# Kernel optimization log

Measured on AMD Instinct MI355X. Metric: run time of the kernel, lower is better.

## Reference

```python
import jax, jax.numpy as jnp
import numpy as np

N = 131072      # total nodes = num_graphs * numNodes
E = 2097152     # edges (avg degree 16)
C_IN = 64
HID = 64        # hiddenChannels
NODES = 128     # numNodes per graph
B = 1024        # num_graphs
NCLS = 4


def setup_inputs() -> dict:
    key = jax.random.key(0)
    ks = jax.random.split(key, 10)
    x = jax.random.normal(ks[0], (N, C_IN), jnp.float32)
    edge_index = jax.random.randint(ks[1], (2, E), 0, N, dtype=jnp.int32)
    edge_attr = jax.random.uniform(ks[2], (E,), jnp.float32)
    # GCNConv params (stored as [in, out]); PyG uses glorot init, bias zeros
    W1 = jax.random.normal(ks[3], (C_IN, 2 * HID), jnp.float32) * (1.0 / np.sqrt(C_IN))
    b1 = jnp.zeros((2 * HID,), jnp.float32)
    W2 = jax.random.normal(ks[4], (2 * HID, HID), jnp.float32) * (1.0 / np.sqrt(2 * HID))
    b2 = jnp.zeros((HID,), jnp.float32)
    Wfc = jax.random.normal(ks[5], (HID * NODES, NCLS), jnp.float32) * (1.0 / np.sqrt(HID * NODES))
    bfc = jnp.zeros((NCLS,), jnp.float32)
    return {"x": x, "edge_index": edge_index, "edge_attr": edge_attr,
            "W1": W1, "b1": b1, "W2": W2, "b2": b2, "Wfc": Wfc, "bfc": bfc}


def gcn_conv(x, src, dst, ew, W, b):
    # PyG GCNConv: add self-loops (weight 1), symmetric normalization,
    # linear transform, scatter-add aggregation at target nodes, + bias.
    loop = jnp.arange(N, dtype=src.dtype)
    s = jnp.concatenate([src, loop])
    d = jnp.concatenate([dst, loop])
    w = jnp.concatenate([ew, jnp.ones((N,), ew.dtype)])
    deg = jax.ops.segment_sum(w, d, num_segments=N)                  # [N]
    dis = jnp.where(deg > 0, jax.lax.rsqrt(jnp.maximum(deg, 1e-30)), 0.0)
    norm = dis[s] * w * dis[d]                                       # [E+N]
    h = x @ W                                                        # [N, out]
    msg = h[s] * norm[:, None]                                       # gather + scale
    out = jax.ops.segment_sum(msg, d, num_segments=N)                # scatter-add
    return out + b


def reference(x, edge_index, edge_attr, W1, b1, W2, b2, Wfc, bfc):
    src, dst = edge_index[0], edge_index[1]
    h = jax.nn.relu(gcn_conv(x, src, dst, edge_attr, W1, b1))
    h = jax.nn.relu(gcn_conv(h, src, dst, edge_attr, W2, b2))
    h = h.reshape(B, HID * NODES)
    logits = h @ Wfc + bfc
    return jax.nn.softmax(logits, axis=1)
```

## Files before the change

### kernel.cpp

```cpp
#include <hip/hip_runtime.h>

#define N_NODES 131072
#define NE      2097152
#define CIN     64
#define HID     64
#define H2X     128
#define NODESG  128
#define NGRAPH  1024
#define NCLS    4

#define NBUCK   256
#define NPB     512
#define HBLK    1024
#define EPB     2048
#define DEGSC   1048576.0f
#define DEGMASK ((1ull << 40) - 1)

typedef short bf16x8 __attribute__((ext_vector_type(8)));
typedef float f32x4  __attribute__((ext_vector_type(4)));

__device__ __forceinline__ unsigned short f2b(float f) {
    unsigned int u = __float_as_uint(f);
    return (unsigned short)((u + 0x7fffu + ((u >> 16) & 1u)) >> 16);
}
__device__ __forceinline__ unsigned int pack2(float a, float b) {
    return (unsigned int)f2b(a) | ((unsigned int)f2b(b) << 16);
}
__device__ __forceinline__ float blo(unsigned u) { return __uint_as_float(u << 16); }
__device__ __forceinline__ float bhi(unsigned u) { return __uint_as_float(u & 0xffff0000u); }


__global__ __launch_bounds__(256) void k_wswiz(
        const float* __restrict__ W1, const float* __restrict__ W2,
        unsigned short* __restrict__ wf1, unsigned short* __restrict__ wf2) {
    int tid = threadIdx.x;
    #pragma unroll
    for (int it = 0; it < 4; ++it) {
        int idx = tid + 256 * it;
        int kt = idx >> 9, nt = (idx >> 6) & 7, l = idx & 63;
        int lm = l & 15, lq = l >> 4;
        unsigned pk[4];
        #pragma unroll
        for (int jp = 0; jp < 4; ++jp) {
            float w0 = W1[(kt*32 + lq*8 + 2*jp)     * H2X + nt*16 + lm];
            float w1 = W1[(kt*32 + lq*8 + 2*jp + 1) * H2X + nt*16 + lm];
            pk[jp] = pack2(w0, w1);
        }
        *(uint4*)&wf1[idx * 8] = make_uint4(pk[0], pk[1], pk[2], pk[3]);
    }
    #pragma unroll
    for (int it = 0; it < 4; ++it) {
        int idx = tid + 256 * it;
        int kt = idx >> 8, nt = (idx >> 6) & 3, l = idx & 63;
        int lm = l & 15, lq = l >> 4;
        unsigned pk[4];
        #pragma unroll
        for (int jp = 0; jp < 4; ++jp) {
            float w0 = W2[(kt*32 + lq*8 + 2*jp)     * HID + nt*16 + lm];
            float w1 = W2[(kt*32 + lq*8 + 2*jp + 1) * HID + nt*16 + lm];
            pk[jp] = pack2(w0, w1);
        }
        *(uint4*)&wf2[idx * 8] = make_uint4(pk[0], pk[1], pk[2], pk[3]);
    }
}


__global__ __launch_bounds__(256) void k_hist(const int* __restrict__ dst,
                                              int* __restrict__ hist) {
    __shared__ unsigned bh[NBUCK];
    int t = threadIdx.x;
    bh[t] = 0;
    __syncthreads();
    int base = blockIdx.x * EPB;
    #pragma unroll
    for (int k = 0; k < EPB / 256; ++k) {
        int d = dst[base + t + 256 * k];
        atomicAdd(&bh[d >> 9], 1u);
    }
    __syncthreads();
    hist[t * HBLK + blockIdx.x] = (int)bh[t];
}

__global__ void k_scan1(const int* __restrict__ in, int* __restrict__ out,
                        int* __restrict__ partial) {
    __shared__ int sd[256];
    int t = threadIdx.x;
    int base = blockIdx.x * 512;
    int c0 = in[base + 2*t];
    int c1 = in[base + 2*t + 1];
    int loc = c0 + c1;
    sd[t] = loc;
    __syncthreads();
    for (int off = 1; off < 256; off <<= 1) {
        int v = (t >= off) ? sd[t - off] : 0;
        __syncthreads();
        sd[t] += v;
        __syncthreads();
    }
    int excl = sd[t] - loc;
    out[base + 2*t]     = excl;
    out[base + 2*t + 1] = excl + c0;
    if (t == 255) partial[blockIdx.x] = sd[t];
}

__global__ void k_scan2(int* __restrict__ partial) {
    __shared__ int sd[256];
    int t = threadIdx.x;
    int p0 = partial[2*t], p1 = partial[2*t + 1];
    int loc = p0 + p1;
    sd[t] = loc;
    __syncthreads();
    for (int off = 1; off < 256; off <<= 1) {
        int v = (t >= off) ? sd[t - off] : 0;
        __syncthreads();
        sd[t] += v;
        __syncthreads();
    }
    int excl = sd[t] - loc;
    partial[2*t]     = excl;
    partial[2*t + 1] = excl + p0;
}

__global__ __launch_bounds__(256) void k_scatter(
        const int* __restrict__ src, const int* __restrict__ dst,
        const float* __restrict__ ew, const int* __restrict__ hist,
        const int* __restrict__ partial, unsigned long long* __restrict__ part) {
    __shared__ unsigned lcur[NBUCK];
    int t = threadIdx.x;
    int gi = t * HBLK + blockIdx.x;
    lcur[t] = (unsigned)(hist[gi] + partial[gi >> 9]);
    __syncthreads();
    int base = blockIdx.x * EPB;
    #pragma unroll
    for (int k = 0; k < EPB / 256; ++k) {
        int e = base + t + 256 * k;
        int s = src[e], d = dst[e];
        unsigned w = __float_as_uint(ew[e]);
        unsigned p = atomicAdd(&lcur[d >> 9], 1u);
        part[p] = ((unsigned long long)w << 32) |
                  ((unsigned long long)(unsigned)(d & 511) << 17) |
                  (unsigned long long)(unsigned)s;
    }
}

__global__ __launch_bounds__(256) void k_bucket(
        const unsigned long long* __restrict__ part, const int* __restrict__ hist,
        const int* __restrict__ partial, int2* __restrict__ csr,
        int* __restrict__ rowptr, int* __restrict__ counts, float* __restrict__ dis) {
    __shared__ unsigned long long dc[NPB];
    __shared__ unsigned cnt2[NPB];
    __shared__ int rp[NPB];
    __shared__ int sd[256];
    int t = threadIdx.x, b = blockIdx.x;
    dc[t] = 0; dc[t + 256] = 0;
    cnt2[t] = 0; cnt2[t + 256] = 0;
    __syncthreads();
    int start = hist[b * HBLK] + partial[2 * b];
    int end   = (b == NBUCK - 1) ? NE : (hist[(b + 1) * HBLK] + partial[2 * (b + 1)]);

    for (int j = start + t; j < end; j += 256) {
        unsigned long long p = part[j];
        unsigned dl = (unsigned)(p >> 17) & 511u;
        float w = __uint_as_float((unsigned)(p >> 32));
        atomicAdd(&dc[dl], (1ull << 40) | (unsigned long long)(unsigned)(w * DEGSC));
    }
    __syncthreads();

    unsigned long long d0 = dc[2*t], d1 = dc[2*t + 1];
    int c0 = (int)(d0 >> 40), c1 = (int)(d1 >> 40);
    int loc = c0 + c1;
    sd[t] = loc;
    __syncthreads();
    for (int off = 1; off < 256; off <<= 1) {
        int v = (t >= off) ? sd[t - off] : 0;
        __syncthreads();
        sd[t] += v;
        __syncthreads();
    }
    int excl = sd[t] - loc;
    rp[2*t] = excl; rp[2*t + 1] = excl + c0;

    int n0 = b * NPB;
    rowptr[n0 + 2*t]     = start + excl;
    rowptr[n0 + 2*t + 1] = start + excl + c0;
    counts[n0 + 2*t]     = c0;
    counts[n0 + 2*t + 1] = c1;
    float dg0 = (float)(d0 & DEGMASK) * (1.0f / DEGSC);
    float dg1 = (float)(d1 & DEGMASK) * (1.0f / DEGSC);
    dis[n0 + 2*t]     = rsqrtf(dg0 + 1.0f);
    dis[n0 + 2*t + 1] = rsqrtf(dg1 + 1.0f);
    __syncthreads();

    for (int j = start + t; j < end; j += 256) {
        unsigned long long p = part[j];
        unsigned dl = (unsigned)(p >> 17) & 511u;
        int s = (int)(p & 0x1ffffu);
        unsigned r = atomicAdd(&cnt2[dl], 1u);
        csr[start + rp[dl] + (int)r] = make_int2(s, (int)(unsigned)(p >> 32));
    }
}

__global__ void k_xcast(const float* __restrict__ x, const float* __restrict__ dis,
                        uint2* __restrict__ xb2) {
    int i = blockIdx.x * blockDim.x + threadIdx.x;
    float d = dis[i >> 4];
    float4 v = ((const float4*)x)[i];
    xb2[i] = make_uint2(pack2(d * v.x, d * v.y), pack2(d * v.z, d * v.w));
}


#define GATHER_PAIR(TAB, pA, pB, nA, nB, cmA, cmB, a0,a1,a2,a3, b0,b1,b2,b3, vSA, vSB) \
    {                                                                                  \
        int   sA0 = __shfl(pA.x, qid),      sA1 = __shfl(pA.x, qid + 4);               \
        int   sA2 = __shfl(pA.x, qid + 8),  sA3 = __shfl(pA.x, qid + 12);              \
        float fA0 = __int_as_float(__shfl(pA.y, qid));                                 \
        float fA1 = __int_as_float(__shfl(pA.y, qid + 4));                             \
        float fA2 = __int_as_float(__shfl(pA.y, qid + 8));                             \
        float fA3 = __int_as_float(__shfl(pA.y, qid + 12));                            \
        int   sB0 = __shfl(pB.x, qid),      sB1 = __shfl(pB.x, qid + 4);               \
        int   sB2 = __shfl(pB.x, qid + 8),  sB3 = __shfl(pB.x, qid + 12);              \
        float fB0 = __int_as_float(__shfl(pB.y, qid));                                 \
        float fB1 = __int_as_float(__shfl(pB.y, qid + 4));                             \
        float fB2 = __int_as_float(__shfl(pB.y, qid + 8));                             \
        float fB3 = __int_as_float(__shfl(pB.y, qid + 12));                            \
        uint2 vA0 = TAB[((unsigned)sA0 << 4) | ql];                                    \
        uint2 vA1 = TAB[((unsigned)sA1 << 4) | ql];                                    \
        uint2 vA2 = TAB[((unsigned)sA2 << 4) | ql];                                    \
        uint2 vA3 = TAB[((unsigned)sA3 << 4) | ql];                                    \
        uint2 vB0 = TAB[((unsigned)sB0 << 4) | ql];                                    \
        uint2 vB1 = TAB[((unsigned)sB1 << 4) | ql];                                    \
        uint2 vB2 = TAB[((unsigned)sB2 << 4) | ql];                                    \
        uint2 vB3 = TAB[((unsigned)sB3 << 4) | ql];                                    \
        vSA = TAB[((unsigned)nA << 4) | ql];                                           \
        vSB = TAB[((unsigned)nB << 4) | ql];                                           \
        a0 = fmaf(fA0, blo(vA0.x), a0); a1 = fmaf(fA0, bhi(vA0.x), a1);                \
        a2 = fmaf(fA0, blo(vA0.y), a2); a3 = fmaf(fA0, bhi(vA0.y), a3);                \
        a0 = fmaf(fA1, blo(vA1.x), a0); a1 = fmaf(fA1, bhi(vA1.x), a1);                \
        a2 = fmaf(fA1, blo(vA1.y), a2); a3 = fmaf(fA1, bhi(vA1.y), a3);                \
        a0 = fmaf(fA2, blo(vA2.x), a0); a1 = fmaf(fA2, bhi(vA2.x), a1);                \
        a2 = fmaf(fA2, blo(vA2.y), a2); a3 = fmaf(fA2, bhi(vA2.y), a3);                \
        a0 = fmaf(fA3, blo(vA3.x), a0); a1 = fmaf(fA3, bhi(vA3.x), a1);                \
        a2 = fmaf(fA3, blo(vA3.y), a2); a3 = fmaf(fA3, bhi(vA3.y), a3);                \
        b0 = fmaf(fB0, blo(vB0.x), b0); b1 = fmaf(fB0, bhi(vB0.x), b1);                \
        b2 = fmaf(fB0, blo(vB0.y), b2); b3 = fmaf(fB0, bhi(vB0.y), b3);                \
        b0 = fmaf(fB1, blo(vB1.x), b0); b1 = fmaf(fB1, bhi(vB1.x), b1);                \
        b2 = fmaf(fB1, blo(vB1.y), b2); b3 = fmaf(fB1, bhi(vB1.y), b3);                \
        b0 = fmaf(fB2, blo(vB2.x), b0); b1 = fmaf(fB2, bhi(vB2.x), b1);                \
        b2 = fmaf(fB2, blo(vB2.y), b2); b3 = fmaf(fB2, bhi(vB2.y), b3);                \
        b0 = fmaf(fB3, blo(vB3.x), b0); b1 = fmaf(fB3, bhi(vB3.x), b1);                \
        b2 = fmaf(fB3, blo(vB3.y), b2); b3 = fmaf(fB3, bhi(vB3.y), b3);                \
        int tsA = (cmA > 16) ? ((cmA - 13) >> 2) : 0;                                  \
        for (int k = 0; k < tsA; ++k) {                                                \
            int jj = 16 + 4 * k + qid;                                                 \
            int   s = __shfl(pA.x, jj);                                                \
            float f = __int_as_float(__shfl(pA.y, jj));                                \
            uint2 v = TAB[((unsigned)s << 4) | ql];                                    \
            a0 = fmaf(f, blo(v.x), a0); a1 = fmaf(f, bhi(v.x), a1);                    \
            a2 = fmaf(f, blo(v.y), a2); a3 = fmaf(f, bhi(v.y), a3);                    \
        }                                                                              \
        int tsB = (cmB > 16) ? ((cmB - 13) >> 2) : 0;                                  \
        for (int k = 0; k < tsB; ++k) {                                                \
            int jj = 16 + 4 * k + qid;                                                 \
            int   s = __shfl(pB.x, jj);                                                \
            float f = __int_as_float(__shfl(pB.y, jj));                                \
            uint2 v = TAB[((unsigned)s << 4) | ql];                                    \
            b0 = fmaf(f, blo(v.x), b0); b1 = fmaf(f, bhi(v.x), b1);                    \
            b2 = fmaf(f, blo(v.y), b2); b3 = fmaf(f, bhi(v.y), b3);                    \
        }                                                                              \
        a0 += __shfl_xor(a0, 16); a1 += __shfl_xor(a1, 16);                            \
        a2 += __shfl_xor(a2, 16); a3 += __shfl_xor(a3, 16);                            \
        a0 += __shfl_xor(a0, 32); a1 += __shfl_xor(a1, 32);                            \
        a2 += __shfl_xor(a2, 32); a3 += __shfl_xor(a3, 32);                            \
        b0 += __shfl_xor(b0, 16); b1 += __shfl_xor(b1, 16);                            \
        b2 += __shfl_xor(b2, 16); b3 += __shfl_xor(b3, 16);                            \
        b0 += __shfl_xor(b0, 32); b1 += __shfl_xor(b1, 32);                            \
        b2 += __shfl_xor(b2, 32); b3 += __shfl_xor(b3, 32);                            \
    }


__global__ __launch_bounds__(256, 4) void k_layer1(
        const uint2* __restrict__ xb2, const int2* __restrict__ csr,
        const int* __restrict__ rowptr, const int* __restrict__ counts,
        const float* __restrict__ dis, const unsigned short* __restrict__ wf1,
        const unsigned short* __restrict__ wf2, const float* __restrict__ b1,
        unsigned short* __restrict__ t2u) {
    __shared__ unsigned short sagg_b[32][72];
    __shared__ unsigned short sh1[32][136];
    __shared__ float sb[H2X];
    int tid = threadIdx.x;
    if (tid < H2X) sb[tid] = b1[tid];

    int wave = tid >> 6, lane = tid & 63;
    int qid = lane >> 4, ql = lane & 15;
    int n0 = blockIdx.x * 32;
    int nb = n0 + wave * 8;

    int cm8[8], cnt8[8], rs8[8];
    float dn8[8];
    int2 myp[8];
    #pragma unroll
    for (int i = 0; i < 8; ++i) {
        rs8[i] = rowptr[nb + i];
        cnt8[i] = counts[nb + i];
        dn8[i] = dis[nb + i];
        cm8[i] = cnt8[i] < 64 ? cnt8[i] : 64;
    }
    #pragma unroll
    for (int i = 0; i < 8; ++i)
        myp[i] = (lane < cm8[i]) ? csr[rs8[i] + lane] : make_int2(0, 0);

    #pragma unroll
    for (int ip = 0; ip < 8; ip += 2) {
        int2 pA = myp[ip], pB = myp[ip + 1];
        int nA = nb + ip, nB = nA + 1;
        float a0 = 0.f, a1 = 0.f, a2 = 0.f, a3 = 0.f;
        float b0 = 0.f, b1v = 0.f, b2v = 0.f, b3 = 0.f;
        uint2 vSA, vSB;
        GATHER_PAIR(xb2, pA, pB, nA, nB, cm8[ip], cm8[ip + 1],
                    a0, a1, a2, a3, b0, b1v, b2v, b3, vSA, vSB);
        for (int jj = 64; jj < cnt8[ip]; ++jj) {
            int2 p = csr[rs8[ip] + jj];
            float f = __int_as_float(p.y);
            uint2 v = xb2[((unsigned)p.x << 4) | ql];
            if (qid == 0) {
                a0 += f * blo(v.x); a1 += f * bhi(v.x);
                a2 += f * blo(v.y); a3 += f * bhi(v.y);
            }
        }
        for (int jj = 64; jj < cnt8[ip + 1]; ++jj) {
            int2 p = csr[rs8[ip + 1] + jj];
            float f = __int_as_float(p.y);
            uint2 v = xb2[((unsigned)p.x << 4) | ql];
            if (qid == 0) {
                b0 += f * blo(v.x); b1v += f * bhi(v.x);
                b2v += f * blo(v.y); b3 += f * bhi(v.y);
            }
        }
        if (qid == 0) {
            float dnA = dn8[ip], dnB = dn8[ip + 1];
            int m = wave * 8 + ip;
            *(uint2*)&sagg_b[m][ql * 4] =
                make_uint2(pack2(dnA * (a0 + blo(vSA.x)), dnA * (a1 + bhi(vSA.x))),
                           pack2(dnA * (a2 + blo(vSA.y)), dnA * (a3 + bhi(vSA.y))));
            *(uint2*)&sagg_b[m + 1][ql * 4] =
                make_uint2(pack2(dnB * (b0 + blo(vSB.x)), dnB * (b1v + bhi(vSB.x))),
                           pack2(dnB * (b2v + blo(vSB.y)), dnB * (b3 + bhi(vSB.y))));
        }
    }
    __syncthreads();

    int mt = wave & 1, ntb = (wave >> 1) * 4;
    int lm = lane & 15, lq = lane >> 4;
    bf16x8 af0 = *(const bf16x8*)&sagg_b[mt*16 + lm][lq * 8];
    bf16x8 af1 = *(const bf16x8*)&sagg_b[mt*16 + lm][32 + lq * 8];
    #pragma unroll
    for (int t = 0; t < 4; ++t) {
        int nt = ntb + t;
        bf16x8 bf0 = *(const bf16x8*)&wf1[(nt*64 + lane) * 8];
        bf16x8 bf1 = *(const bf16x8*)&wf1[((8 + nt)*64 + lane) * 8];
        f32x4 acc = {0.f, 0.f, 0.f, 0.f};
        acc = __builtin_amdgcn_mfma_f32_16x16x32_bf16(af0, bf0, acc, 0, 0, 0);
        acc = __builtin_amdgcn_mfma_f32_16x16x32_bf16(af1, bf1, acc, 0, 0, 0);
        int ch = nt*16 + lm;
        float bias = sb[ch];
        #pragma unroll
        for (int r = 0; r < 4; ++r)
            sh1[mt*16 + lq*4 + r][ch] = f2b(fmaxf(acc[r] + bias, 0.f));
    }
    __syncthreads();

    #pragma unroll
    for (int ti = 0; ti < 2; ++ti) {
        int t = wave * 2 + ti;
        int mt2 = t & 1, nt2 = t >> 1;
        f32x4 acc = {0.f, 0.f, 0.f, 0.f};
        #pragma unroll
        for (int kt = 0; kt < 4; ++kt) {
            bf16x8 af = *(const bf16x8*)&sh1[mt2*16 + lm][kt*32 + lq*8];
            bf16x8 bf = *(const bf16x8*)&wf2[((kt*4 + nt2)*64 + lane) * 8];
            acc = __builtin_amdgcn_mfma_f32_16x16x32_bf16(af, bf, acc, 0, 0, 0);
        }
        int ch = nt2*16 + lm;
        #pragma unroll
        for (int r = 0; r < 4; ++r) {
            int node = n0 + mt2*16 + lq*4 + r;
            t2u[(size_t)node * HID + ch] = f2b(dis[node] * acc[r]);
        }
    }
}


__global__ __launch_bounds__(256, 4) void k_agg2(
        const uint2* __restrict__ t2y, const int2* __restrict__ csr,
        const int* __restrict__ rowptr, const int* __restrict__ counts,
        const float* __restrict__ dis, const float* __restrict__ b2,
        unsigned short* __restrict__ h2b) {
    int tid = threadIdx.x;
    int wave = tid >> 6, lane = tid & 63;
    int qid = lane >> 4, ql = lane & 15;
    float4 bb = *(const float4*)&b2[ql * 4];
    int n0 = blockIdx.x * 32;
    int nb = n0 + wave * 8;

    int cm8[8], cnt8[8], rs8[8];
    float dn8[8];
    int2 myp[8];
    #pragma unroll
    for (int i = 0; i < 8; ++i) {
        rs8[i] = rowptr[nb + i];
        cnt8[i] = counts[nb + i];
        dn8[i] = dis[nb + i];
        cm8[i] = cnt8[i] < 64 ? cnt8[i] : 64;
    }
    #pragma unroll
    for (int i = 0; i < 8; ++i)
        myp[i] = (lane < cm8[i]) ? csr[rs8[i] + lane] : make_int2(0, 0);

    #pragma unroll
    for (int ip = 0; ip < 8; ip += 2) {
        int2 pA = myp[ip], pB = myp[ip + 1];
        int nA = nb + ip, nB = nA + 1;
        float a0 = 0.f, a1 = 0.f, a2 = 0.f, a3 = 0.f;
        float b0 = 0.f, b1v = 0.f, b2v = 0.f, b3 = 0.f;
        uint2 vSA, vSB;
        GATHER_PAIR(t2y, pA, pB, nA, nB, cm8[ip], cm8[ip + 1],
                    a0, a1, a2, a3, b0, b1v, b2v, b3, vSA, vSB);
        for (int jj = 64; jj < cnt8[ip]; ++jj) {
            int2 p = csr[rs8[ip] + jj];
            float f = __int_as_float(p.y);
            uint2 v = t2y[((unsigned)p.x << 4) | ql];
            if (qid == 0) {
                a0 += f * blo(v.x); a1 += f * bhi(v.x);
                a2 += f * blo(v.y); a3 += f * bhi(v.y);
            }
        }
        for (int jj = 64; jj < cnt8[ip + 1]; ++jj) {
            int2 p = csr[rs8[ip + 1] + jj];
            float f = __int_as_float(p.y);
            uint2 v = t2y[((unsigned)p.x << 4) | ql];
            if (qid == 0) {
                b0 += f * blo(v.x); b1v += f * bhi(v.x);
                b2v += f * blo(v.y); b3 += f * bhi(v.y);
            }
        }
        if (qid == 0) {
            float dnA = dn8[ip], dnB = dn8[ip + 1];
            float oa0 = fmaxf(fmaf(dnA, a0 + blo(vSA.x), bb.x), 0.f);
            float oa1 = fmaxf(fmaf(dnA, a1 + bhi(vSA.x), bb.y), 0.f);
            float oa2 = fmaxf(fmaf(dnA, a2 + blo(vSA.y), bb.z), 0.f);
            float oa3 = fmaxf(fmaf(dnA, a3 + bhi(vSA.y), bb.w), 0.f);
            float ob0 = fmaxf(fmaf(dnB, b0 + blo(vSB.x), bb.x), 0.f);
            float ob1 = fmaxf(fmaf(dnB, b1v + bhi(vSB.x), bb.y), 0.f);
            float ob2 = fmaxf(fmaf(dnB, b2v + blo(vSB.y), bb.z), 0.f);
            float ob3 = fmaxf(fmaf(dnB, b3 + bhi(vSB.y), bb.w), 0.f);
            *(uint2*)&h2b[((unsigned)nA << 6) | (ql * 4)] =
                make_uint2(pack2(oa0, oa1), pack2(oa2, oa3));
            *(uint2*)&h2b[((unsigned)nB << 6) | (ql * 4)] =
                make_uint2(pack2(ob0, ob1), pack2(ob2, ob3));
        }
    }
}


__global__ __launch_bounds__(256) void k_fc(
        const unsigned short* __restrict__ h2b, const float* __restrict__ Wfc,
        const float* __restrict__ bfc, float* __restrict__ out) {
    __shared__ float4 red[256];
    int b = blockIdx.x, t = threadIdx.x;
    const uint2* hrow = (const uint2*)(h2b + (size_t)b * (HID * NODESG));
    const float4* W4 = (const float4*)Wfc;
    float4 a = make_float4(0.f, 0.f, 0.f, 0.f);
    #pragma unroll
    for (int j = 0; j < 8; ++j) {
        int i = j * 256 + t;
        uint2 hv = hrow[i];
        float h0 = blo(hv.x), h1 = bhi(hv.x), h2v = blo(hv.y), h3 = bhi(hv.y);
        float4 w0 = W4[i * 4 + 0];
        float4 w1 = W4[i * 4 + 1];
        float4 w2 = W4[i * 4 + 2];
        float4 w3 = W4[i * 4 + 3];
        a.x = fmaf(h0, w0.x, a.x); a.y = fmaf(h0, w0.y, a.y);
        a.z = fmaf(h0, w0.z, a.z); a.w = fmaf(h0, w0.w, a.w);
        a.x = fmaf(h1, w1.x, a.x); a.y = fmaf(h1, w1.y, a.y);
        a.z = fmaf(h1, w1.z, a.z); a.w = fmaf(h1, w1.w, a.w);
        a.x = fmaf(h2v, w2.x, a.x); a.y = fmaf(h2v, w2.y, a.y);
        a.z = fmaf(h2v, w2.z, a.z); a.w = fmaf(h2v, w2.w, a.w);
        a.x = fmaf(h3, w3.x, a.x); a.y = fmaf(h3, w3.y, a.y);
        a.z = fmaf(h3, w3.z, a.z); a.w = fmaf(h3, w3.w, a.w);
    }
    red[t] = a;
    __syncthreads();
    for (int s = 128; s > 0; s >>= 1) {
        if (t < s) {
            red[t].x += red[t + s].x; red[t].y += red[t + s].y;
            red[t].z += red[t + s].z; red[t].w += red[t + s].w;
        }
        __syncthreads();
    }
    if (t == 0) {
        float l0 = red[0].x + bfc[0];
        float l1 = red[0].y + bfc[1];
        float l2 = red[0].z + bfc[2];
        float l3 = red[0].w + bfc[3];
        float mx = fmaxf(fmaxf(l0, l1), fmaxf(l2, l3));
        float e0 = expf(l0 - mx), e1 = expf(l1 - mx);
        float e2 = expf(l2 - mx), e3 = expf(l3 - mx);
        float inv = 1.f / (e0 + e1 + e2 + e3);
        float4 o = make_float4(e0 * inv, e1 * inv, e2 * inv, e3 * inv);
        *(float4*)&out[(size_t)b * 4] = o;
    }
}


extern "C" void kernel_launch(void* const* d_in, const int* in_sizes, int n_in,
                              void* d_out, int out_size, void* d_ws, size_t ws_size,
                              hipStream_t stream) {
    const float* x   = (const float*)d_in[0];
    const int*   ei  = (const int*)  d_in[1];
    const float* ea  = (const float*)d_in[2];
    const float* W1  = (const float*)d_in[3];
    const float* b1  = (const float*)d_in[4];
    const float* W2  = (const float*)d_in[5];
    const float* b2  = (const float*)d_in[6];
    const float* Wfc = (const float*)d_in[7];
    const float* bfc = (const float*)d_in[8];
    float* out = (float*)d_out;
    const int* src = ei;
    const int* dst = ei + NE;

    char* ws = (char*)d_ws;
    size_t off = 0;
    int*   hist   = (int*)  (ws + off); off += (size_t)NBUCK * HBLK * 4;
    int*   partial= (int*)  (ws + off); off += 4096;
    int*   counts = (int*)  (ws + off); off += (size_t)N_NODES * 4;
    int*   rowptr = (int*)  (ws + off); off += (size_t)N_NODES * 4;
    float* dis    = (float*)(ws + off); off += (size_t)N_NODES * 4;
    unsigned short* wf1 = (unsigned short*)(ws + off); off += 8192 * 2;
    unsigned short* wf2 = (unsigned short*)(ws + off); off += 8192 * 2;
    int2*  csr    = (int2*) (ws + off); off += (size_t)NE * 8;
    uint2* xb2    = (uint2*)(ws + off); off += (size_t)N_NODES * CIN * 2;
    unsigned short* t2u = (unsigned short*)(ws + off); off += (size_t)N_NODES * HID * 2;
    unsigned short* h2b = (unsigned short*)(ws + off); off += (size_t)N_NODES * HID * 2;
    unsigned long long* part = (unsigned long long*)t2u;

    hipMemsetAsync(hist, 0, (size_t)NBUCK * HBLK * 4 + 4096, stream);

    k_wswiz  <<<1, 256, 0, stream>>>(W1, W2, wf1, wf2);
    k_hist   <<<HBLK, 256, 0, stream>>>(dst, hist);
    k_scan1  <<<NBUCK * HBLK / 512, 256, 0, stream>>>(hist, hist, partial);
    k_scan2  <<<1, 256, 0, stream>>>(partial);
    k_scatter<<<HBLK, 256, 0, stream>>>(src, dst, ea, hist, partial, part);
    k_bucket <<<NBUCK, 256, 0, stream>>>(part, hist, partial, csr, rowptr, counts, dis);
    k_xcast  <<<(N_NODES * CIN / 4) / 256, 256, 0, stream>>>(x, dis, xb2);
    k_layer1 <<<N_NODES / 32, 256, 0, stream>>>(xb2, csr, rowptr, counts, dis,
                                                wf1, wf2, b1, t2u);
    k_agg2   <<<N_NODES / 32, 256, 0, stream>>>((const uint2*)t2u, csr, rowptr,
                                                counts, dis, b2, h2b);
    k_fc     <<<NGRAPH, 256, 0, stream>>>(h2b, Wfc, bfc, out);
}
```

Baseline: 267.4 us.

## Software-pipeline neighbor gathers across node pairs in aggregation kernels

```diff
diff --git a/kernel.cpp b/kernel.cpp
--- a/kernel.cpp
+++ b/kernel.cpp
@@ -209,72 +209,49 @@
 }
 
 
-#define GATHER_PAIR(TAB, pA, pB, nA, nB, cmA, cmB, a0,a1,a2,a3, b0,b1,b2,b3, vSA, vSB) \
-    {                                                                                  \
-        int   sA0 = __shfl(pA.x, qid),      sA1 = __shfl(pA.x, qid + 4);               \
-        int   sA2 = __shfl(pA.x, qid + 8),  sA3 = __shfl(pA.x, qid + 12);              \
-        float fA0 = __int_as_float(__shfl(pA.y, qid));                                 \
-        float fA1 = __int_as_float(__shfl(pA.y, qid + 4));                             \
-        float fA2 = __int_as_float(__shfl(pA.y, qid + 8));                             \
-        float fA3 = __int_as_float(__shfl(pA.y, qid + 12));                            \
-        int   sB0 = __shfl(pB.x, qid),      sB1 = __shfl(pB.x, qid + 4);               \
-        int   sB2 = __shfl(pB.x, qid + 8),  sB3 = __shfl(pB.x, qid + 12);              \
-        float fB0 = __int_as_float(__shfl(pB.y, qid));                                 \
-        float fB1 = __int_as_float(__shfl(pB.y, qid + 4));                             \
-        float fB2 = __int_as_float(__shfl(pB.y, qid + 8));                             \
-        float fB3 = __int_as_float(__shfl(pB.y, qid + 12));                            \
-        uint2 vA0 = TAB[((unsigned)sA0 << 4) | ql];                                    \
-        uint2 vA1 = TAB[((unsigned)sA1 << 4) | ql];                                    \
-        uint2 vA2 = TAB[((unsigned)sA2 << 4) | ql];                                    \
-        uint2 vA3 = TAB[((unsigned)sA3 << 4) | ql];                                    \
-        uint2 vB0 = TAB[((unsigned)sB0 << 4) | ql];                                    \
-        uint2 vB1 = TAB[((unsigned)sB1 << 4) | ql];                                    \
-        uint2 vB2 = TAB[((unsigned)sB2 << 4) | ql];                                    \
-        uint2 vB3 = TAB[((unsigned)sB3 << 4) | ql];                                    \
-        vSA = TAB[((unsigned)nA << 4) | ql];                                           \
-        vSB = TAB[((unsigned)nB << 4) | ql];                                           \
-        a0 = fmaf(fA0, blo(vA0.x), a0); a1 = fmaf(fA0, bhi(vA0.x), a1);                \
-        a2 = fmaf(fA0, blo(vA0.y), a2); a3 = fmaf(fA0, bhi(vA0.y), a3);                \
-        a0 = fmaf(fA1, blo(vA1.x), a0); a1 = fmaf(fA1, bhi(vA1.x), a1);                \
-        a2 = fmaf(fA1, blo(vA1.y), a2); a3 = fmaf(fA1, bhi(vA1.y), a3);                \
-        a0 = fmaf(fA2, blo(vA2.x), a0); a1 = fmaf(fA2, bhi(vA2.x), a1);                \
-        a2 = fmaf(fA2, blo(vA2.y), a2); a3 = fmaf(fA2, bhi(vA2.y), a3);                \
-        a0 = fmaf(fA3, blo(vA3.x), a0); a1 = fmaf(fA3, bhi(vA3.x), a1);                \
-        a2 = fmaf(fA3, blo(vA3.y), a2); a3 = fmaf(fA3, bhi(vA3.y), a3);                \
-        b0 = fmaf(fB0, blo(vB0.x), b0); b1 = fmaf(fB0, bhi(vB0.x), b1);                \
-        b2 = fmaf(fB0, blo(vB0.y), b2); b3 = fmaf(fB0, bhi(vB0.y), b3);                \
-        b0 = fmaf(fB1, blo(vB1.x), b0); b1 = fmaf(fB1, bhi(vB1.x), b1);                \
-        b2 = fmaf(fB1, blo(vB1.y), b2); b3 = fmaf(fB1, bhi(vB1.y), b3);                \
-        b0 = fmaf(fB2, blo(vB2.x), b0); b1 = fmaf(fB2, bhi(vB2.x), b1);                \
-        b2 = fmaf(fB2, blo(vB2.y), b2); b3 = fmaf(fB2, bhi(vB2.y), b3);                \
-        b0 = fmaf(fB3, blo(vB3.x), b0); b1 = fmaf(fB3, bhi(vB3.x), b1);                \
-        b2 = fmaf(fB3, blo(vB3.y), b2); b3 = fmaf(fB3, bhi(vB3.y), b3);                \
-        int tsA = (cmA > 16) ? ((cmA - 13) >> 2) : 0;                                  \
-        for (int k = 0; k < tsA; ++k) {                                                \
-            int jj = 16 + 4 * k + qid;                                                 \
-            int   s = __shfl(pA.x, jj);                                                \
-            float f = __int_as_float(__shfl(pA.y, jj));                                \
-            uint2 v = TAB[((unsigned)s << 4) | ql];                                    \
-            a0 = fmaf(f, blo(v.x), a0); a1 = fmaf(f, bhi(v.x), a1);                    \
-            a2 = fmaf(f, blo(v.y), a2); a3 = fmaf(f, bhi(v.y), a3);                    \
-        }                                                                              \
-        int tsB = (cmB > 16) ? ((cmB - 13) >> 2) : 0;                                  \
-        for (int k = 0; k < tsB; ++k) {                                                \
-            int jj = 16 + 4 * k + qid;                                                 \
-            int   s = __shfl(pB.x, jj);                                                \
-            float f = __int_as_float(__shfl(pB.y, jj));                                \
-            uint2 v = TAB[((unsigned)s << 4) | ql];                                    \
-            b0 = fmaf(f, blo(v.x), b0); b1 = fmaf(f, bhi(v.x), b1);                    \
-            b2 = fmaf(f, blo(v.y), b2); b3 = fmaf(f, bhi(v.y), b3);                    \
-        }                                                                              \
-        a0 += __shfl_xor(a0, 16); a1 += __shfl_xor(a1, 16);                            \
-        a2 += __shfl_xor(a2, 16); a3 += __shfl_xor(a3, 16);                            \
-        a0 += __shfl_xor(a0, 32); a1 += __shfl_xor(a1, 32);                            \
-        a2 += __shfl_xor(a2, 32); a3 += __shfl_xor(a3, 32);                            \
-        b0 += __shfl_xor(b0, 16); b1 += __shfl_xor(b1, 16);                            \
-        b2 += __shfl_xor(b2, 16); b3 += __shfl_xor(b3, 16);                            \
-        b0 += __shfl_xor(b0, 32); b1 += __shfl_xor(b1, 32);                            \
-        b2 += __shfl_xor(b2, 32); b3 += __shfl_xor(b3, 32);                            \
+struct G4 { uint2 v0, v1, v2, v3; };
+
+__device__ __forceinline__ G4 issue4(const uint2* __restrict__ TAB, int2 p,
+                                     int base, int qid, int ql) {
+    int s0 = __shfl(p.x, base + qid);
+    int s1 = __shfl(p.x, base + qid + 4);
+    int s2 = __shfl(p.x, base + qid + 8);
+    int s3 = __shfl(p.x, base + qid + 12);
+    G4 g;
+    g.v0 = TAB[((unsigned)s0 << 4) | ql];
+    g.v1 = TAB[((unsigned)s1 << 4) | ql];
+    g.v2 = TAB[((unsigned)s2 << 4) | ql];
+    g.v3 = TAB[((unsigned)s3 << 4) | ql];
+    return g;
+}
+
+__device__ __forceinline__ void consume4(const G4& g, int2 p, int base, int qid,
+                                         float& x0, float& x1, float& x2, float& x3) {
+    float f0 = __int_as_float(__shfl(p.y, base + qid));
+    float f1 = __int_as_float(__shfl(p.y, base + qid + 4));
+    float f2 = __int_as_float(__shfl(p.y, base + qid + 8));
+    float f3 = __int_as_float(__shfl(p.y, base + qid + 12));
+    x0 = fmaf(f0, blo(g.v0.x), x0); x1 = fmaf(f0, bhi(g.v0.x), x1);
+    x2 = fmaf(f0, blo(g.v0.y), x2); x3 = fmaf(f0, bhi(g.v0.y), x3);
+    x0 = fmaf(f1, blo(g.v1.x), x0); x1 = fmaf(f1, bhi(g.v1.x), x1);
+    x2 = fmaf(f1, blo(g.v1.y), x2); x3 = fmaf(f1, bhi(g.v1.y), x3);
+    x0 = fmaf(f2, blo(g.v2.x), x0); x1 = fmaf(f2, bhi(g.v2.x), x1);
+    x2 = fmaf(f2, blo(g.v2.y), x2); x3 = fmaf(f2, bhi(g.v2.y), x3);
+    x0 = fmaf(f3, blo(g.v3.x), x0); x1 = fmaf(f3, bhi(g.v3.x), x1);
+    x2 = fmaf(f3, blo(g.v3.y), x2); x3 = fmaf(f3, bhi(g.v3.y), x3);
+}
+
+#define TAIL32(TAB, pp, cm, x0, x1, x2, x3)                                    \
+    if (cm > 32) {                                                             \
+        int ts = (cm - 29) >> 2;                                               \
+        for (int k = 0; k < ts; ++k) {                                         \
+            int jj = 32 + 4 * k + qid;                                         \
+            int   s = __shfl(pp.x, jj);                                        \
+            float f = __int_as_float(__shfl(pp.y, jj));                        \
+            uint2 v = TAB[((unsigned)s << 4) | ql];                            \
+            x0 = fmaf(f, blo(v.x), x0); x1 = fmaf(f, bhi(v.x), x1);            \
+            x2 = fmaf(f, blo(v.y), x2); x3 = fmaf(f, bhi(v.y), x3);            \
+        }                                                                      \
     }
 
 
@@ -295,50 +272,79 @@
     int n0 = blockIdx.x * 32;
     int nb = n0 + wave * 8;
 
-    int cm8[8], cnt8[8], rs8[8];
+    int cnt8[8];
     float dn8[8];
     int2 myp[8];
     #pragma unroll
     for (int i = 0; i < 8; ++i) {
-        rs8[i] = rowptr[nb + i];
-        cnt8[i] = counts[nb + i];
+        int rs = rowptr[nb + i];
+        int c = counts[nb + i];
+        cnt8[i] = c;
         dn8[i] = dis[nb + i];
-        cm8[i] = cnt8[i] < 64 ? cnt8[i] : 64;
-    }
-    #pragma unroll
-    for (int i = 0; i < 8; ++i)
-        myp[i] = (lane < cm8[i]) ? csr[rs8[i] + lane] : make_int2(0, 0);
-
-    #pragma unroll
-    for (int ip = 0; ip < 8; ip += 2) {
-        int2 pA = myp[ip], pB = myp[ip + 1];
-        int nA = nb + ip, nB = nA + 1;
+        int cm = c < 64 ? c : 64;
+        myp[i] = (lane < cm) ? csr[rs + lane] : make_int2(0, 0);
+    }
+
+    G4 mA = issue4(xb2, myp[0], 0, qid, ql);
+    G4 mB = issue4(xb2, myp[1], 0, qid, ql);
+    #pragma unroll
+    for (int ip = 0; ip < 4; ++ip) {
+        const int iA = 2 * ip, iB = iA + 1;
+        int nA = nb + iA, nB = nb + iB;
+        G4 cA = issue4(xb2, myp[iA], 16, qid, ql);
+        G4 cB = issue4(xb2, myp[iB], 16, qid, ql);
+        uint2 vSA = xb2[((unsigned)nA << 4) | ql];
+        uint2 vSB = xb2[((unsigned)nB << 4) | ql];
+        G4 nxA, nxB;
+        if (ip < 3) {
+            nxA = issue4(xb2, myp[iA + 2], 0, qid, ql);
+            nxB = issue4(xb2, myp[iB + 2], 0, qid, ql);
+        }
         float a0 = 0.f, a1 = 0.f, a2 = 0.f, a3 = 0.f;
         float b0 = 0.f, b1v = 0.f, b2v = 0.f, b3 = 0.f;
-        uint2 vSA, vSB;
-        GATHER_PAIR(xb2, pA, pB, nA, nB, cm8[ip], cm8[ip + 1],
-                    a0, a1, a2, a3, b0, b1v, b2v, b3, vSA, vSB);
-        for (int jj = 64; jj < cnt8[ip]; ++jj) {
-            int2 p = csr[rs8[ip] + jj];
-            float f = __int_as_float(p.y);
-            uint2 v = xb2[((unsigned)p.x << 4) | ql];
-            if (qid == 0) {
-                a0 += f * blo(v.x); a1 += f * bhi(v.x);
-                a2 += f * blo(v.y); a3 += f * bhi(v.y);
+        consume4(mA, myp[iA], 0, qid, a0, a1, a2, a3);
+        consume4(mB, myp[iB], 0, qid, b0, b1v, b2v, b3);
+        consume4(cA, myp[iA], 16, qid, a0, a1, a2, a3);
+        consume4(cB, myp[iB], 16, qid, b0, b1v, b2v, b3);
+        int cmA = cnt8[iA] < 64 ? cnt8[iA] : 64;
+        int cmB = cnt8[iB] < 64 ? cnt8[iB] : 64;
+        TAIL32(xb2, myp[iA], cmA, a0, a1, a2, a3);
+        TAIL32(xb2, myp[iB], cmB, b0, b1v, b2v, b3);
+        a0 += __shfl_xor(a0, 16); a1 += __shfl_xor(a1, 16);
+        a2 += __shfl_xor(a2, 16); a3 += __shfl_xor(a3, 16);
+        a0 += __shfl_xor(a0, 32); a1 += __shfl_xor(a1, 32);
+        a2 += __shfl_xor(a2, 32); a3 += __shfl_xor(a3, 32);
+        b0 += __shfl_xor(b0, 16); b1v += __shfl_xor(b1v, 16);
+        b2v += __shfl_xor(b2v, 16); b3 += __shfl_xor(b3, 16);
+        b0 += __shfl_xor(b0, 32); b1v += __shfl_xor(b1v, 32);
+        b2v += __shfl_xor(b2v, 32); b3 += __shfl_xor(b3, 32);
+        if (cnt8[iA] > 64) {
+            int rs = rowptr[nA];
+            for (int jj = 64; jj < cnt8[iA]; ++jj) {
+                int2 p = csr[rs + jj];
+                float f = __int_as_float(p.y);
+                uint2 v = xb2[((unsigned)p.x << 4) | ql];
+                if (qid == 0) {
+                    a0 += f * blo(v.x); a1 += f * bhi(v.x);
+                    a2 += f * blo(v.y); a3 += f * bhi(v.y);
+                }
             }
         }
-        for (int jj = 64; jj < cnt8[ip + 1]; ++jj) {
-            int2 p = csr[rs8[ip + 1] + jj];
-            float f = __int_as_float(p.y);
-            uint2 v = xb2[((unsigned)p.x << 4) | ql];
-            if (qid == 0) {
-                b0 += f * blo(v.x); b1v += f * bhi(v.x);
-                b2v += f * blo(v.y); b3 += f * bhi(v.y);
+        if (cnt8[iB] > 64) {
+            int rs = rowptr[nB];
+            for (int jj = 64; jj < cnt8[iB]; ++jj) {
+                int2 p = csr[rs + jj];
+                float f = __int_as_float(p.y);
+                uint2 v = xb2[((unsigned)p.x << 4) | ql];
+                if (qid == 0) {
+                    b0 += f * blo(v.x); b1v += f * bhi(v.x);
+                    b2v += f * blo(v.y); b3 += f * bhi(v.y);
+                }
             }
         }
         if (qid == 0) {
-            float dnA = dn8[ip], dnB = dn8[ip + 1];
-            int m = wave * 8 + ip;
+            float dnA = dn8[iA], dnB = dn8[iB];
+            int m = wave * 8 + iA;
             *(uint2*)&sagg_b[m][ql * 4] =
                 make_uint2(pack2(dnA * (a0 + blo(vSA.x)), dnA * (a1 + bhi(vSA.x))),
                            pack2(dnA * (a2 + blo(vSA.y)), dnA * (a3 + bhi(vSA.y))));
@@ -346,6 +352,7 @@
                 make_uint2(pack2(dnB * (b0 + blo(vSB.x)), dnB * (b1v + bhi(vSB.x))),
                            pack2(dnB * (b2v + blo(vSB.y)), dnB * (b3 + bhi(vSB.y))));
         }
+        if (ip < 3) { mA = nxA; mB = nxB; }
     }
     __syncthreads();
 
@@ -402,49 +409,78 @@
     int n0 = blockIdx.x * 32;
     int nb = n0 + wave * 8;
 
-    int cm8[8], cnt8[8], rs8[8];
+    int cnt8[8];
     float dn8[8];
     int2 myp[8];
     #pragma unroll
     for (int i = 0; i < 8; ++i) {
-        rs8[i] = rowptr[nb + i];
-        cnt8[i] = counts[nb + i];
+        int rs = rowptr[nb + i];
+        int c = counts[nb + i];
+        cnt8[i] = c;
         dn8[i] = dis[nb + i];
-        cm8[i] = cnt8[i] < 64 ? cnt8[i] : 64;
-    }
-    #pragma unroll
-    for (int i = 0; i < 8; ++i)
-        myp[i] = (lane < cm8[i]) ? csr[rs8[i] + lane] : make_int2(0, 0);
-
-    #pragma unroll
-    for (int ip = 0; ip < 8; ip += 2) {
-        int2 pA = myp[ip], pB = myp[ip + 1];
-        int nA = nb + ip, nB = nA + 1;
+        int cm = c < 64 ? c : 64;
+        myp[i] = (lane < cm) ? csr[rs + lane] : make_int2(0, 0);
+    }
+
+    G4 mA = issue4(t2y, myp[0], 0, qid, ql);
+    G4 mB = issue4(t2y, myp[1], 0, qid, ql);
+    #pragma unroll
+    for (int ip = 0; ip < 4; ++ip) {
+        const int iA = 2 * ip, iB = iA + 1;
+        int nA = nb + iA, nB = nb + iB;
+        G4 cA = issue4(t2y, myp[iA], 16, qid, ql);
+        G4 cB = issue4(t2y, myp[iB], 16, qid, ql);
+        uint2 vSA = t2y[((unsigned)nA << 4) | ql];
+        uint2 vSB = t2y[((unsigned)nB << 4) | ql];
+        G4 nxA, nxB;
+        if (ip < 3) {
+            nxA = issue4(t2y, myp[iA + 2], 0, qid, ql);
+            nxB = issue4(t2y, myp[iB + 2], 0, qid, ql);
+        }
         float a0 = 0.f, a1 = 0.f, a2 = 0.f, a3 = 0.f;
         float b0 = 0.f, b1v = 0.f, b2v = 0.f, b3 = 0.f;
-        uint2 vSA, vSB;
-        GATHER_PAIR(t2y, pA, pB, nA, nB, cm8[ip], cm8[ip + 1],
-                    a0, a1, a2, a3, b0, b1v, b2v, b3, vSA, vSB);
-        for (int jj = 64; jj < cnt8[ip]; ++jj) {
-            int2 p = csr[rs8[ip] + jj];
-            float f = __int_as_float(p.y);
-            uint2 v = t2y[((unsigned)p.x << 4) | ql];
-            if (qid == 0) {
-                a0 += f * blo(v.x); a1 += f * bhi(v.x);
-                a2 += f * blo(v.y); a3 += f * bhi(v.y);
+        consume4(mA, myp[iA], 0, qid, a0, a1, a2, a3);
+        consume4(mB, myp[iB], 0, qid, b0, b1v, b2v, b3);
+        consume4(cA, myp[iA], 16, qid, a0, a1, a2, a3);
+        consume4(cB, myp[iB], 16, qid, b0, b1v, b2v, b3);
+        int cmA = cnt8[iA] < 64 ? cnt8[iA] : 64;
+        int cmB = cnt8[iB] < 64 ? cnt8[iB] : 64;
+        TAIL32(t2y, myp[iA], cmA, a0, a1, a2, a3);
+        TAIL32(t2y, myp[iB], cmB, b0, b1v, b2v, b3);
+        a0 += __shfl_xor(a0, 16); a1 += __shfl_xor(a1, 16);
+        a2 += __shfl_xor(a2, 16); a3 += __shfl_xor(a3, 16);
+        a0 += __shfl_xor(a0, 32); a1 += __shfl_xor(a1, 32);
+        a2 += __shfl_xor(a2, 32); a3 += __shfl_xor(a3, 32);
+        b0 += __shfl_xor(b0, 16); b1v += __shfl_xor(b1v, 16);
+        b2v += __shfl_xor(b2v, 16); b3 += __shfl_xor(b3, 16);
+        b0 += __shfl_xor(b0, 32); b1v += __shfl_xor(b1v, 32);
+        b2v += __shfl_xor(b2v, 32); b3 += __shfl_xor(b3, 32);
+        if (cnt8[iA] > 64) {
+            int rs = rowptr[nA];
+            for (int jj = 64; jj < cnt8[iA]; ++jj) {
+                int2 p = csr[rs + jj];
+                float f = __int_as_float(p.y);
+                uint2 v = t2y[((unsigned)p.x << 4) | ql];
+                if (qid == 0) {
+                    a0 += f * blo(v.x); a1 += f * bhi(v.x);
+                    a2 += f * blo(v.y); a3 += f * bhi(v.y);
+                }
             }
         }
-        for (int jj = 64; jj < cnt8[ip + 1]; ++jj) {
-            int2 p = csr[rs8[ip + 1] + jj];
-            float f = __int_as_float(p.y);
-            uint2 v = t2y[((unsigned)p.x << 4) | ql];
-            if (qid == 0) {
-                b0 += f * blo(v.x); b1v += f * bhi(v.x);
-                b2v += f * blo(v.y); b3 += f * bhi(v.y);
+        if (cnt8[iB] > 64) {
+            int rs = rowptr[nB];
+            for (int jj = 64; jj < cnt8[iB]; ++jj) {
+                int2 p = csr[rs + jj];
+                float f = __int_as_float(p.y);
+                uint2 v = t2y[((unsigned)p.x << 4) | ql];
+                if (qid == 0) {
+                    b0 += f * blo(v.x); b1v += f * bhi(v.x);
+                    b2v += f * blo(v.y); b3 += f * bhi(v.y);
+                }
             }
         }
         if (qid == 0) {
-            float dnA = dn8[ip], dnB = dn8[ip + 1];
+            float dnA = dn8[iA], dnB = dn8[iB];
             float oa0 = fmaxf(fmaf(dnA, a0 + blo(vSA.x), bb.x), 0.f);
             float oa1 = fmaxf(fmaf(dnA, a1 + bhi(vSA.x), bb.y), 0.f);
             float oa2 = fmaxf(fmaf(dnA, a2 + blo(vSA.y), bb.z), 0.f);
@@ -458,6 +494,7 @@
             *(uint2*)&h2b[((unsigned)nB << 6) | (ql * 4)] =
                 make_uint2(pack2(ob0, ob1), pack2(ob2, ob3));
         }
+        if (ip < 3) { mA = nxA; mB = nxB; }
     }
 }
 
```

Measured after the change: 311.4 us. +16.4%, slower.
